# Kernel optimization log

Measured on AMD Instinct MI355X. Metric: run time of the kernel, lower is better.

Reference implementation:

```python
import jax, jax.numpy as jnp
import numpy as np

V, B, T, D, H = 32000, 64, 256, 512, 1024


def setup_inputs() -> dict:
    key = jax.random.key(0)
    ks = jax.random.split(key, 8)
    s = lambda i, shape: (jax.random.normal(ks[i], shape, jnp.float32) * 0.02)
    return {
        "y": jax.random.randint(ks[0], (B, T), 0, V),
        "hidden": jnp.zeros((B, H), jnp.float32),
        "emb_table": s(1, (V, D)),
        "Wx": s(2, (D, 3 * H)),
        "Wh": s(3, (H, 3 * H)),
        "bx": jnp.zeros((3 * H,), jnp.float32),
        "bh": jnp.zeros((3 * H,), jnp.float32),
        "W_out": s(4, (H, D)),
        "b_out": jnp.zeros((D,), jnp.float32),
    }


def _gru_step(h, x, Wx, Wh, bx, bh):
    # PyTorch GRUCell semantics: r,z gates, candidate n with r gating the
    # recurrent contribution (including its bias term).
    gx = x @ Wx + bx          # [B, 3H]
    gh = h @ Wh + bh          # [B, 3H]
    xr, xz, xn = jnp.split(gx, 3, axis=-1)
    hr, hz, hn = jnp.split(gh, 3, axis=-1)
    r = jax.nn.sigmoid(xr + hr)
    z = jax.nn.sigmoid(xz + hz)
    n = jnp.tanh(xn + r * hn)
    return (1.0 - z) * n + z * h


def reference(y, hidden, emb_table, Wx, Wh, bx, bh, W_out, b_out):
    emb = emb_table[y]                       # [B, T, D] token embedding lookup

    def step(h, x_t):                        # x_t: [B, D]
        h2 = _gru_step(h, x_t, Wx, Wh, bx, bh)
        return h2, h2

    _, outs = jax.lax.scan(step, hidden, jnp.swapaxes(emb, 0, 1))  # [T, B, H]
    out = jnp.swapaxes(outs, 0, 1)           # [B, T, H] decoder hiddens
    logits = jnp.tanh(out @ W_out + b_out)   # [B, T, D]; dropout_rate=0 -> identity
    return logits
```

## Files before the change

### kernel.cpp

```cpp
#include <hip/hip_runtime.h>
#include <stdint.h>

typedef unsigned short u16;
typedef unsigned int u32;
typedef __attribute__((ext_vector_type(4))) unsigned int u32x4;
typedef __attribute__((ext_vector_type(4))) float f32x4;
typedef __attribute__((ext_vector_type(8))) __bf16 bf16x8;

#define MFMA16(a, b, c) __builtin_amdgcn_mfma_f32_16x16x32_bf16((a), (b), (c), 0, 0, 0)

__device__ __forceinline__ u16 f2b(float f) {
  union { float f; unsigned u; } v; v.f = f;
  unsigned r = v.u + 0x7FFFu + ((v.u >> 16) & 1u);
  return (u16)(r >> 16);
}
__device__ __forceinline__ float b2f(u16 h) {
  union { unsigned u; float f; } v; v.u = ((unsigned)h) << 16;
  return v.f;
}
__device__ __forceinline__ float sigm(float x) { return 1.0f / (1.0f + __expf(-x)); }
__device__ __forceinline__ float tanh_fast(float x) {
  x = fminf(fmaxf(x, -15.0f), 15.0f);
  float t = __expf(2.0f * x);
  return (t - 1.0f) / (t + 1.0f);
}

template <int OFF>
__device__ __forceinline__ u32x4 ld16_sc(const void* p) {
  u32x4 r;
  asm volatile("global_load_dwordx4 %0, %1, off offset:%2 sc0 sc1"
               : "=v"(r) : "v"(p), "i"(OFF));
  return r;
}
__device__ __forceinline__ void st16_sc(void* p, u32x4 v) {
  asm volatile("global_store_dwordx4 %0, %1, off sc0 sc1"
               :: "v"(p), "v"(v) : "memory");
}
__device__ __forceinline__ void st4_sc(u32* p, u32 v) {
  asm volatile("global_store_dword %0, %1, off sc0 sc1"
               :: "v"(p), "v"(v) : "memory");
}
__device__ __forceinline__ u32 ld4_sc(const u32* p) {
  u32 r;
  asm volatile("global_load_dword %0, %1, off sc0 sc1\n\t"
               "s_waitcnt vmcnt(0)"
               : "=v"(r) : "v"(p) : "memory");
  return r;
}


__global__ void transpose_cvt(const float* __restrict__ src, u16* __restrict__ dst,
                              int R, int C) {
  __shared__ float tile[32][33];
  const int c0 = blockIdx.x * 32, r0 = blockIdx.y * 32;
  const int tx = threadIdx.x, ty = threadIdx.y;
  for (int i = ty; i < 32; i += 8)
    tile[i][tx] = src[(size_t)(r0 + i) * C + (c0 + tx)];
  __syncthreads();
  for (int i = ty; i < 32; i += 8)
    dst[(size_t)(c0 + i) * R + (r0 + tx)] = f2b(tile[tx][i]);
}

__global__ void gather_cast(const int* __restrict__ y, const float* __restrict__ tab,
                            u16* __restrict__ A) {
  const int idx = blockIdx.x * 256 + threadIdx.x;
  const int m = idx >> 7;
  const int d0 = (idx & 127) << 2;
  const float4 v = *reinterpret_cast<const float4*>(tab + (size_t)y[m] * 512 + d0);
  ushort4 o;
  o.x = f2b(v.x); o.y = f2b(v.y); o.z = f2b(v.z); o.w = f2b(v.w);
  *reinterpret_cast<ushort4*>(A + (size_t)m * 512 + d0) = o;
}

__global__ void cast_h0_blocked(const float* __restrict__ h, u16* __restrict__ dst) {
  const int i = blockIdx.x * 256 + threadIdx.x;
  const int b = i >> 10, n = i & 1023;
  const int r = b >> 4, ii = b & 15, g = n >> 4, j = n & 15;
  dst[((size_t)r * 64 + g) * 256 + ii * 16 + j] = f2b(h[(size_t)b * 1024 + n]);
}

template <int EPI>
__global__ __launch_bounds__(256, 2) void gemm_bt(
    const u16* __restrict__ A, const u16* __restrict__ Bt,
    const float* __restrict__ bias, void* __restrict__ Cout,
    int M, int N, int K) {
  __shared__ u16 As[4096], Bs[4096];
  const int tid = threadIdx.x, lane = tid & 63, w = tid >> 6;
  const int wm = w >> 1, wn = w & 1, c = lane & 15, hq = lane >> 4;
  const int m0 = blockIdx.y * 128, n0 = blockIdx.x * 128;
  f32x4 acc[4][4] = {};

  const int slot0 = tid, slot1 = 256 + tid;
  const int r0_ = slot0 >> 2, ko0 = (slot0 & 3) << 3;
  const int r1_ = slot1 >> 2, ko1 = (slot1 & 3) << 3;

  for (int k0 = 0; k0 < K; k0 += 32) {
    const u32x4 a0 = *(const u32x4*)(A + (size_t)(m0 + r0_) * K + k0 + ko0);
    const u32x4 a1 = *(const u32x4*)(A + (size_t)(m0 + r1_) * K + k0 + ko1);
    const u32x4 b0 = *(const u32x4*)(Bt + (size_t)(n0 + r0_) * K + k0 + ko0);
    const u32x4 b1 = *(const u32x4*)(Bt + (size_t)(n0 + r1_) * K + k0 + ko1);
    __syncthreads();
    *(u32x4*)(As + r0_ * 32 + ko0) = a0;
    *(u32x4*)(As + r1_ * 32 + ko1) = a1;
    *(u32x4*)(Bs + r0_ * 32 + ko0) = b0;
    *(u32x4*)(Bs + r1_ * 32 + ko1) = b1;
    __syncthreads();
    u32x4 af[4], bf[4];
#pragma unroll
    for (int i = 0; i < 4; ++i) {
      af[i] = *(const u32x4*)(As + (wm * 64 + i * 16 + c) * 32 + hq * 8);
      bf[i] = *(const u32x4*)(Bs + (wn * 64 + i * 16 + c) * 32 + hq * 8);
    }
#pragma unroll
    for (int mi = 0; mi < 4; ++mi)
#pragma unroll
      for (int ni = 0; ni < 4; ++ni)
        acc[mi][ni] = MFMA16(__builtin_bit_cast(bf16x8, af[mi]),
                             __builtin_bit_cast(bf16x8, bf[ni]), acc[mi][ni]);
  }

#pragma unroll
  for (int ni = 0; ni < 4; ++ni) {
    const int col = n0 + wn * 64 + ni * 16 + c;
    const float bv = bias[col];
#pragma unroll
    for (int mi = 0; mi < 4; ++mi) {
#pragma unroll
      for (int i = 0; i < 4; ++i) {
        const int m = m0 + wm * 64 + mi * 16 + hq * 4 + i;
        const float v = acc[mi][ni][i] + bv;
        if (EPI == 0) {
          const int dr = (m & 255) * 64 + (m >> 8);
          ((u16*)Cout)[(size_t)dr * N + col] = f2b(v);
        } else {
          const int dr = (m & 63) * 256 + (m >> 6);
          ((float*)Cout)[(size_t)dr * N + col] = tanh_fast(v);
        }
      }
    }
  }
}

__global__ __launch_bounds__(320, 1) void scan_kernel(
    const u16* __restrict__ wh_t,
    const float* __restrict__ bh,
    const float* __restrict__ h0,
    const u16* __restrict__ gx,
    u16* __restrict__ hbuf,
    u16* __restrict__ outs,
    u32* __restrict__ tags) {
  __shared__ u16 whs[96 * 512];
  __shared__ float red[2][4][3][256];
  __shared__ __align__(16) u16 htile[16][16];
  const int g = blockIdx.x >> 2, r = blockIdx.x & 3;
  const int tid = threadIdx.x, lane = tid & 63, s = tid >> 6;
  const int c = lane & 15, hq = lane >> 4;
  const int gcol = g * 16 + c;
  const int row0 = r * 16;

  for (int fb = s; fb < 96; fb += 5) {
    const int ss = fb / 24, kk = (fb % 24) / 3, ct = fb % 3;
    const int n = ct * 1024 + g * 16 + c;
    const int k = ss * 256 + kk * 32 + hq * 8;
    *(u32x4*)(whs + fb * 512 + lane * 8) =
        *(const u32x4*)(wh_t + (size_t)n * 1024 + k);
  }
  float bhv[3], hprev[4];
  u16 gxr[4][3];
  if (s == 4) {
#pragma unroll
    for (int ct = 0; ct < 3; ++ct) bhv[ct] = bh[ct * 1024 + gcol];
#pragma unroll
    for (int i = 0; i < 4; ++i)
      hprev[i] = h0[(size_t)(row0 + hq * 4 + i) * 1024 + gcol];
    const u16* gp = gx + gcol;
#pragma unroll
    for (int i = 0; i < 4; ++i) {
      const int b = row0 + hq * 4 + i;
      gxr[i][0] = gp[(size_t)b * 3072];
      gxr[i][1] = gp[(size_t)b * 3072 + 1024];
      gxr[i][2] = gp[(size_t)b * 3072 + 2048];
    }
  }
  __syncthreads();

  for (int t = 0; t < 256; ++t) {
    if (s < 4) {
      if (t > 0 && lane < 16) {
        const u32* tp = tags + (((size_t)(t & 1) * 4 + r) * 64 + s * 16 + lane) * 32;
        while (__ballot(ld4_sc(tp) < (u32)t)) {}
      }

      u32x4 af[8];
      {
        const u16* ap0 = hbuf + (((size_t)(t & 1) * 4 + r) * 64 + s * 16 + (hq >> 1)) * 256 +
                         c * 16 + (hq & 1) * 8;
        const u16* ap1 = ap0 + 2048;
        af[0] = ld16_sc<0>(ap0);    af[1] = ld16_sc<1024>(ap0);
        af[2] = ld16_sc<2048>(ap0); af[3] = ld16_sc<3072>(ap0);
        af[4] = ld16_sc<0>(ap1);    af[5] = ld16_sc<1024>(ap1);
        af[6] = ld16_sc<2048>(ap1); af[7] = ld16_sc<3072>(ap1);
      }
      asm volatile("s_waitcnt vmcnt(0)" ::: "memory");
      __builtin_amdgcn_sched_barrier(0);

      f32x4 acc[3] = {};
#pragma unroll
      for (int kk = 0; kk < 8; ++kk) {
        const int fb = (s * 8 + kk) * 3;
        const u32x4 b0 = *(const u32x4*)(whs + (fb + 0) * 512 + lane * 8);
        const u32x4 b1 = *(const u32x4*)(whs + (fb + 1) * 512 + lane * 8);
        const u32x4 b2 = *(const u32x4*)(whs + (fb + 2) * 512 + lane * 8);
        const bf16x8 a = __builtin_bit_cast(bf16x8, af[kk]);
        acc[0] = MFMA16(a, __builtin_bit_cast(bf16x8, b0), acc[0]);
        acc[1] = MFMA16(a, __builtin_bit_cast(bf16x8, b1), acc[1]);
        acc[2] = MFMA16(a, __builtin_bit_cast(bf16x8, b2), acc[2]);
      }
#pragma unroll
      for (int ct = 0; ct < 3; ++ct)
        *(f32x4*)&red[t & 1][s][ct][lane * 4] = acc[ct];
    }
    __syncthreads();

    if (s == 4) {
      f32x4 a0 = {}, a1 = {}, a2 = {};
#pragma unroll
      for (int j = 0; j < 4; ++j) {
        a0 += *(const f32x4*)&red[t & 1][j][0][lane * 4];
        a1 += *(const f32x4*)&red[t & 1][j][1][lane * 4];
        a2 += *(const f32x4*)&red[t & 1][j][2][lane * 4];
      }
#pragma unroll
      for (int i = 0; i < 4; ++i) {
        const float xr = b2f(gxr[i][0]);
        const float xz = b2f(gxr[i][1]);
        const float xn = b2f(gxr[i][2]);
        const float rr = sigm(xr + a0[i] + bhv[0]);
        const float zz = sigm(xz + a1[i] + bhv[1]);
        const float nn = tanh_fast(xn + rr * (a2[i] + bhv[2]));
        const float hnew = (1.0f - zz) * nn + zz * hprev[i];
        hprev[i] = hnew;
        htile[hq * 4 + i][c] = f2b(hnew);
      }
      asm volatile("s_waitcnt lgkmcnt(0)" ::: "memory");
      __builtin_amdgcn_sched_barrier(0);
      u32x4 hv;
      if (lane < 32) {
        hv = *(const u32x4*)((const u16*)htile + lane * 8);
        st16_sc(hbuf + (((size_t)((t + 1) & 1) * 4 + r) * 64 + g) * 256 + lane * 8, hv);
      }
      asm volatile("s_waitcnt vmcnt(0)" ::: "memory");
      if (lane == 0)
        st4_sc(tags + (((size_t)((t + 1) & 1) * 4 + r) * 64 + g) * 32, (u32)(t + 1));
      if (lane < 32) {
        const int row = row0 + (lane >> 1), c8 = (lane & 1) * 8;
        *(u32x4*)(outs + ((size_t)t * 64 + row) * 1024 + g * 16 + c8) = hv;
      }
      if (t < 255) {
        const u16* gp = gx + (size_t)(t + 1) * 64 * 3072 + gcol;
#pragma unroll
        for (int i = 0; i < 4; ++i) {
          const int b = row0 + hq * 4 + i;
          gxr[i][0] = gp[(size_t)b * 3072];
          gxr[i][1] = gp[(size_t)b * 3072 + 1024];
          gxr[i][2] = gp[(size_t)b * 3072 + 2048];
        }
      }
    }
  }
}

extern "C" void kernel_launch(void* const* d_in, const int* in_sizes, int n_in,
                              void* d_out, int out_size, void* d_ws, size_t ws_size,
                              hipStream_t stream) {
  (void)in_sizes; (void)n_in; (void)out_size; (void)ws_size;
  const int* y = (const int*)d_in[0];
  const float* hidden = (const float*)d_in[1];
  const float* emb = (const float*)d_in[2];
  const float* Wx = (const float*)d_in[3];
  const float* Wh = (const float*)d_in[4];
  const float* bx = (const float*)d_in[5];
  const float* bh = (const float*)d_in[6];
  const float* Wout = (const float*)d_in[7];
  const float* bout = (const float*)d_in[8];

  char* p = (char*)d_ws;
  u16* wx_t = (u16*)p; p += (size_t)3072 * 512 * 2;
  u16* wh_t = (u16*)p; p += (size_t)3072 * 1024 * 2;
  u16* wo_t = (u16*)p; p += (size_t)512 * 1024 * 2;
  u16* aemb = (u16*)p; p += (size_t)16384 * 512 * 2;
  u16* gx   = (u16*)p; p += (size_t)16384 * 3072 * 2;
  u16* outs = (u16*)p; p += (size_t)16384 * 1024 * 2;
  u16* hbuf = (u16*)p; p += (size_t)2 * 4 * 64 * 256 * 2;
  u32* tags = (u32*)p;

  hipMemsetAsync(tags, 0, 2 * 4 * 64 * 32 * sizeof(u32), stream);
  transpose_cvt<<<dim3(96, 16), dim3(32, 8), 0, stream>>>(Wx, wx_t, 512, 3072);
  transpose_cvt<<<dim3(96, 32), dim3(32, 8), 0, stream>>>(Wh, wh_t, 1024, 3072);
  transpose_cvt<<<dim3(16, 32), dim3(32, 8), 0, stream>>>(Wout, wo_t, 1024, 512);
  gather_cast<<<dim3(8192), dim3(256), 0, stream>>>(y, emb, aemb);
  cast_h0_blocked<<<dim3(256), dim3(256), 0, stream>>>(hidden, hbuf);

  gemm_bt<0><<<dim3(24, 128), dim3(256), 0, stream>>>(aemb, wx_t, bx, (void*)gx,
                                                      16384, 3072, 512);
  scan_kernel<<<dim3(256), dim3(320), 0, stream>>>(wh_t, bh, hidden, gx,
                                                   hbuf, outs, tags);
  gemm_bt<1><<<dim3(4, 128), dim3(256), 0, stream>>>(outs, wo_t, bout,
                                                     d_out, 16384, 512, 1024);
}
```

Before: 934.8 us.

## Keep full hidden history in blocked hbuf, drop separate outs copy, pipeline tag polling

The scan now writes each step's hidden state to a per-timestep slot in a 257-deep blocked buffer instead of a double buffer. This removes the extra row-major store to outs, and the output GEMM reads the blocked layout directly through a new A-layout template path. Tag polling keeps two outstanding loads in flight, and h-tile reads use plain loads instead of cache-bypassing asm loads. The cost is a larger workspace and a more complex address computation in the output GEMM. Plain loads may return stale cached data, although each slot is written only once.

```diff
diff --git a/kernel.cpp b/kernel.cpp
--- a/kernel.cpp
+++ b/kernel.cpp
@@ -25,13 +25,6 @@
   return (t - 1.0f) / (t + 1.0f);
 }
 
-template <int OFF>
-__device__ __forceinline__ u32x4 ld16_sc(const void* p) {
-  u32x4 r;
-  asm volatile("global_load_dwordx4 %0, %1, off offset:%2 sc0 sc1"
-               : "=v"(r) : "v"(p), "i"(OFF));
-  return r;
-}
 __device__ __forceinline__ void st16_sc(void* p, u32x4 v) {
   asm volatile("global_store_dwordx4 %0, %1, off sc0 sc1"
                :: "v"(p), "v"(v) : "memory");
@@ -39,13 +32,6 @@
 __device__ __forceinline__ void st4_sc(u32* p, u32 v) {
   asm volatile("global_store_dword %0, %1, off sc0 sc1"
                :: "v"(p), "v"(v) : "memory");
-}
-__device__ __forceinline__ u32 ld4_sc(const u32* p) {
-  u32 r;
-  asm volatile("global_load_dword %0, %1, off sc0 sc1\n\t"
-               "s_waitcnt vmcnt(0)"
-               : "=v"(r) : "v"(p) : "memory");
-  return r;
 }
 
 
@@ -79,7 +65,7 @@
   dst[((size_t)r * 64 + g) * 256 + ii * 16 + j] = f2b(h[(size_t)b * 1024 + n]);
 }
 
-template <int EPI>
+template <int EPI, int ALAYOUT>
 __global__ __launch_bounds__(256, 2) void gemm_bt(
     const u16* __restrict__ A, const u16* __restrict__ Bt,
     const float* __restrict__ bias, void* __restrict__ Cout,
@@ -95,8 +81,17 @@
   const int r1_ = slot1 >> 2, ko1 = (slot1 & 3) << 3;
 
   for (int k0 = 0; k0 < K; k0 += 32) {
-    const u32x4 a0 = *(const u32x4*)(A + (size_t)(m0 + r0_) * K + k0 + ko0);
-    const u32x4 a1 = *(const u32x4*)(A + (size_t)(m0 + r1_) * K + k0 + ko1);
+    u32x4 a0, a1;
+    if (ALAYOUT == 0) {
+      a0 = *(const u32x4*)(A + (size_t)(m0 + r0_) * K + k0 + ko0);
+      a1 = *(const u32x4*)(A + (size_t)(m0 + r1_) * K + k0 + ko1);
+    } else {
+      const int ma = m0 + r0_, ka = k0 + ko0, mb = m0 + r1_, kb = k0 + ko1;
+      a0 = *(const u32x4*)(A + ((((size_t)(ma >> 6) + 1) * 4 + ((ma >> 4) & 3)) * 64 +
+                                (ka >> 4)) * 256 + (ma & 15) * 16 + (ka & 15));
+      a1 = *(const u32x4*)(A + ((((size_t)(mb >> 6) + 1) * 4 + ((mb >> 4) & 3)) * 64 +
+                                (kb >> 4)) * 256 + (mb & 15) * 16 + (kb & 15));
+    }
     const u32x4 b0 = *(const u32x4*)(Bt + (size_t)(n0 + r0_) * K + k0 + ko0);
     const u32x4 b1 = *(const u32x4*)(Bt + (size_t)(n0 + r1_) * K + k0 + ko1);
     __syncthreads();
@@ -147,7 +142,6 @@
     const float* __restrict__ h0,
     const u16* __restrict__ gx,
     u16* __restrict__ hbuf,
-    u16* __restrict__ outs,
     u32* __restrict__ tags) {
   __shared__ u16 whs[96 * 512];
   __shared__ float red[2][4][3][256];
@@ -186,23 +180,37 @@
 
   for (int t = 0; t < 256; ++t) {
     if (s < 4) {
-      if (t > 0 && lane < 16) {
-        const u32* tp = tags + (((size_t)(t & 1) * 4 + r) * 64 + s * 16 + lane) * 32;
-        while (__ballot(ld4_sc(tp) < (u32)t)) {}
+      if (t > 0) {
+        const u32* tp = tags + ((size_t)(t & 1) * 4 + r) * (64 * 32) +
+                        (s * 16 + (lane & 15)) * 32;
+        u32 v0, v1;
+        asm volatile("global_load_dword %0, %1, off sc0 sc1" : "=v"(v0) : "v"(tp));
+        asm volatile("global_load_dword %0, %1, off sc0 sc1" : "=v"(v1) : "v"(tp));
+        while (true) {
+          asm volatile("s_waitcnt vmcnt(1)" ::: "memory");
+          if (!__ballot(v0 < (u32)t)) break;
+          asm volatile("global_load_dword %0, %1, off sc0 sc1" : "=v"(v0) : "v"(tp));
+          asm volatile("s_waitcnt vmcnt(1)" ::: "memory");
+          if (!__ballot(v1 < (u32)t)) break;
+          asm volatile("global_load_dword %0, %1, off sc0 sc1" : "=v"(v1) : "v"(tp));
+        }
+        asm volatile("s_waitcnt vmcnt(0)" ::: "memory");
       }
 
       u32x4 af[8];
       {
-        const u16* ap0 = hbuf + (((size_t)(t & 1) * 4 + r) * 64 + s * 16 + (hq >> 1)) * 256 +
-                         c * 16 + (hq & 1) * 8;
+        const u16* ap0 = hbuf + ((size_t)t * 4 + r) * 16384 +
+                         (s * 16 + (hq >> 1)) * 256 + c * 16 + (hq & 1) * 8;
         const u16* ap1 = ap0 + 2048;
-        af[0] = ld16_sc<0>(ap0);    af[1] = ld16_sc<1024>(ap0);
-        af[2] = ld16_sc<2048>(ap0); af[3] = ld16_sc<3072>(ap0);
-        af[4] = ld16_sc<0>(ap1);    af[5] = ld16_sc<1024>(ap1);
-        af[6] = ld16_sc<2048>(ap1); af[7] = ld16_sc<3072>(ap1);
-      }
-      asm volatile("s_waitcnt vmcnt(0)" ::: "memory");
-      __builtin_amdgcn_sched_barrier(0);
+        af[0] = *(const u32x4*)(ap0);
+        af[1] = *(const u32x4*)(ap0 + 512);
+        af[2] = *(const u32x4*)(ap0 + 1024);
+        af[3] = *(const u32x4*)(ap0 + 1536);
+        af[4] = *(const u32x4*)(ap1);
+        af[5] = *(const u32x4*)(ap1 + 512);
+        af[6] = *(const u32x4*)(ap1 + 1024);
+        af[7] = *(const u32x4*)(ap1 + 1536);
+      }
 
       f32x4 acc[3] = {};
 #pragma unroll
@@ -244,18 +252,14 @@
       }
       asm volatile("s_waitcnt lgkmcnt(0)" ::: "memory");
       __builtin_amdgcn_sched_barrier(0);
-      u32x4 hv;
       if (lane < 32) {
-        hv = *(const u32x4*)((const u16*)htile + lane * 8);
-        st16_sc(hbuf + (((size_t)((t + 1) & 1) * 4 + r) * 64 + g) * 256 + lane * 8, hv);
+        const u32x4 hv = *(const u32x4*)((const u16*)htile + lane * 8);
+        st16_sc(hbuf + ((size_t)(t + 1) * 4 + r) * 16384 + g * 256 + lane * 8, hv);
       }
       asm volatile("s_waitcnt vmcnt(0)" ::: "memory");
       if (lane == 0)
-        st4_sc(tags + (((size_t)((t + 1) & 1) * 4 + r) * 64 + g) * 32, (u32)(t + 1));
-      if (lane < 32) {
-        const int row = row0 + (lane >> 1), c8 = (lane & 1) * 8;
-        *(u32x4*)(outs + ((size_t)t * 64 + row) * 1024 + g * 16 + c8) = hv;
-      }
+        st4_sc(tags + ((size_t)((t + 1) & 1) * 4 + r) * (64 * 32) + g * 32,
+               (u32)(t + 1));
       if (t < 255) {
         const u16* gp = gx + (size_t)(t + 1) * 64 * 3072 + gcol;
 #pragma unroll
@@ -290,8 +294,7 @@
   u16* wo_t = (u16*)p; p += (size_t)512 * 1024 * 2;
   u16* aemb = (u16*)p; p += (size_t)16384 * 512 * 2;
   u16* gx   = (u16*)p; p += (size_t)16384 * 3072 * 2;
-  u16* outs = (u16*)p; p += (size_t)16384 * 1024 * 2;
-  u16* hbuf = (u16*)p; p += (size_t)2 * 4 * 64 * 256 * 2;
+  u16* hbuf = (u16*)p; p += (size_t)257 * 4 * 64 * 256 * 2;
   u32* tags = (u32*)p;
 
   hipMemsetAsync(tags, 0, 2 * 4 * 64 * 32 * sizeof(u32), stream);
@@ -301,10 +304,10 @@
   gather_cast<<<dim3(8192), dim3(256), 0, stream>>>(y, emb, aemb);
   cast_h0_blocked<<<dim3(256), dim3(256), 0, stream>>>(hidden, hbuf);
 
-  gemm_bt<0><<<dim3(24, 128), dim3(256), 0, stream>>>(aemb, wx_t, bx, (void*)gx,
-                                                      16384, 3072, 512);
+  gemm_bt<0, 0><<<dim3(24, 128), dim3(256), 0, stream>>>(aemb, wx_t, bx, (void*)gx,
+                                                         16384, 3072, 512);
   scan_kernel<<<dim3(256), dim3(320), 0, stream>>>(wh_t, bh, hidden, gx,
-                                                   hbuf, outs, tags);
-  gemm_bt<1><<<dim3(4, 128), dim3(256), 0, stream>>>(outs, wo_t, bout,
-                                                     d_out, 16384, 512, 1024);
-}
+                                                   hbuf, tags);
+  gemm_bt<1, 1><<<dim3(4, 128), dim3(256), 0, stream>>>(hbuf, wo_t, bout,
+                                                        d_out, 16384, 512, 1024);
+}
```

Result: slower. 1.057 ms (+13.1%).

## Fuse prep kernels, stream GEMM tiles via global_load_lds, drop outs buffer

Applied to the files above, without the earlier changes.

Merges the three transposes, the embedding gather, the h0 cast and the tag memset into one prep kernel, which removes several launches. The GEMM now copies tiles from global memory straight into LDS with global_load_lds instead of staging them through registers. The scan writes every timestep's hidden state into a 257-slot blocked history buffer rather than a double buffer plus a separate outs array. The output GEMM reads that blocked layout directly, so the extra outs store is gone from the serial recurrence, at the cost of more complex address math and a larger workspace.

```diff
diff --git a/kernel.cpp b/kernel.cpp
--- a/kernel.cpp
+++ b/kernel.cpp
@@ -48,38 +48,61 @@
   return r;
 }
 
-
-__global__ void transpose_cvt(const float* __restrict__ src, u16* __restrict__ dst,
-                              int R, int C) {
+__device__ __forceinline__ void gld_lds16(const void* g, void* l) {
+  __builtin_amdgcn_global_load_lds(
+      (const __attribute__((address_space(1))) void*)(g),
+      (__attribute__((address_space(3))) void*)(l), 16, 0, 0);
+}
+
+__global__ __launch_bounds__(256) void prep_all(
+    const float* __restrict__ Wx, const float* __restrict__ Wh,
+    const float* __restrict__ Wout, const int* __restrict__ y,
+    const float* __restrict__ emb, const float* __restrict__ hidden,
+    u16* __restrict__ wx_t, u16* __restrict__ wh_t, u16* __restrict__ wo_t,
+    u16* __restrict__ aemb, u16* __restrict__ hbuf, u32* __restrict__ tags) {
   __shared__ float tile[32][33];
-  const int c0 = blockIdx.x * 32, r0 = blockIdx.y * 32;
-  const int tx = threadIdx.x, ty = threadIdx.y;
-  for (int i = ty; i < 32; i += 8)
-    tile[i][tx] = src[(size_t)(r0 + i) * C + (c0 + tx)];
-  __syncthreads();
-  for (int i = ty; i < 32; i += 8)
-    dst[(size_t)(c0 + i) * R + (r0 + tx)] = f2b(tile[tx][i]);
-}
-
-__global__ void gather_cast(const int* __restrict__ y, const float* __restrict__ tab,
-                            u16* __restrict__ A) {
-  const int idx = blockIdx.x * 256 + threadIdx.x;
-  const int m = idx >> 7;
-  const int d0 = (idx & 127) << 2;
-  const float4 v = *reinterpret_cast<const float4*>(tab + (size_t)y[m] * 512 + d0);
-  ushort4 o;
-  o.x = f2b(v.x); o.y = f2b(v.y); o.z = f2b(v.z); o.w = f2b(v.w);
-  *reinterpret_cast<ushort4*>(A + (size_t)m * 512 + d0) = o;
-}
-
-__global__ void cast_h0_blocked(const float* __restrict__ h, u16* __restrict__ dst) {
-  const int i = blockIdx.x * 256 + threadIdx.x;
-  const int b = i >> 10, n = i & 1023;
-  const int r = b >> 4, ii = b & 15, g = n >> 4, j = n & 15;
-  dst[((size_t)r * 64 + g) * 256 + ii * 16 + j] = f2b(h[(size_t)b * 1024 + n]);
-}
-
-template <int EPI>
+  const int b = blockIdx.x, tid = threadIdx.x;
+  const int tx = tid & 31, ty = tid >> 5;
+
+  const float* src = nullptr; u16* dst = nullptr; int R = 0, C = 0, tb = 0;
+  if (b < 1536)      { src = Wx;   dst = wx_t; R = 512;  C = 3072; tb = b; }
+  else if (b < 4608) { src = Wh;   dst = wh_t; R = 1024; C = 3072; tb = b - 1536; }
+  else if (b < 5120) { src = Wout; dst = wo_t; R = 1024; C = 512;  tb = b - 4608; }
+
+  if (src) {
+    const int xt = C >> 5;
+    const int c0 = (tb % xt) * 32, r0 = (tb / xt) * 32;
+    for (int i = ty; i < 32; i += 8)
+      tile[i][tx] = src[(size_t)(r0 + i) * C + (c0 + tx)];
+    __syncthreads();
+    for (int i = ty; i < 32; i += 8)
+      dst[(size_t)(c0 + i) * R + (r0 + tx)] = f2b(tile[tx][i]);
+    return;
+  }
+  if (b < 13312) {
+    const int idx = (b - 5120) * 256 + tid;
+    const int m = idx >> 7, d0 = (idx & 127) << 2;
+    const float4 v = *reinterpret_cast<const float4*>(emb + (size_t)y[m] * 512 + d0);
+    ushort4 o;
+    o.x = f2b(v.x); o.y = f2b(v.y); o.z = f2b(v.z); o.w = f2b(v.w);
+    *reinterpret_cast<ushort4*>(aemb + (size_t)m * 512 + d0) = o;
+    return;
+  }
+  if (b < 13568) {
+    const int i = (b - 13312) * 256 + tid;
+    const int bb = i >> 10, n = i & 1023;
+    const int r = bb >> 4, ii = bb & 15, g = n >> 4, j = n & 15;
+    hbuf[((size_t)r * 64 + g) * 256 + ii * 16 + j] = f2b(hidden[(size_t)bb * 1024 + n]);
+    return;
+  }
+  {
+    const int base = ((b - 13568) * 256 + tid) * 8;
+#pragma unroll
+    for (int q = 0; q < 8; ++q) tags[base + q] = 0;
+  }
+}
+
+template <int EPI, int ALAYOUT>
 __global__ __launch_bounds__(256, 2) void gemm_bt(
     const u16* __restrict__ A, const u16* __restrict__ Bt,
     const float* __restrict__ bias, void* __restrict__ Cout,
@@ -90,20 +113,28 @@
   const int m0 = blockIdx.y * 128, n0 = blockIdx.x * 128;
   f32x4 acc[4][4] = {};
 
-  const int slot0 = tid, slot1 = 256 + tid;
-  const int r0_ = slot0 >> 2, ko0 = (slot0 & 3) << 3;
-  const int r1_ = slot1 >> 2, ko1 = (slot1 & 3) << 3;
+  const int r0_ = tid >> 2, ko0 = (tid & 3) << 3;
+  const int r1_ = (256 + tid) >> 2, ko1 = ((256 + tid) & 3) << 3;
 
   for (int k0 = 0; k0 < K; k0 += 32) {
-    const u32x4 a0 = *(const u32x4*)(A + (size_t)(m0 + r0_) * K + k0 + ko0);
-    const u32x4 a1 = *(const u32x4*)(A + (size_t)(m0 + r1_) * K + k0 + ko1);
-    const u32x4 b0 = *(const u32x4*)(Bt + (size_t)(n0 + r0_) * K + k0 + ko0);
-    const u32x4 b1 = *(const u32x4*)(Bt + (size_t)(n0 + r1_) * K + k0 + ko1);
+    const u16 *ga0, *ga1;
+    if (ALAYOUT == 0) {
+      ga0 = A + (size_t)(m0 + r0_) * K + k0 + ko0;
+      ga1 = A + (size_t)(m0 + r1_) * K + k0 + ko1;
+    } else {
+      const int ma = m0 + r0_, ka = k0 + ko0, mb = m0 + r1_, kb = k0 + ko1;
+      ga0 = A + ((((size_t)(ma >> 6) + 1) * 4 + ((ma >> 4) & 3)) * 64 +
+                 (ka >> 4)) * 256 + (ma & 15) * 16 + (ka & 15);
+      ga1 = A + ((((size_t)(mb >> 6) + 1) * 4 + ((mb >> 4) & 3)) * 64 +
+                 (kb >> 4)) * 256 + (mb & 15) * 16 + (kb & 15);
+    }
+    const u16* gb0 = Bt + (size_t)(n0 + r0_) * K + k0 + ko0;
+    const u16* gb1 = Bt + (size_t)(n0 + r1_) * K + k0 + ko1;
     __syncthreads();
-    *(u32x4*)(As + r0_ * 32 + ko0) = a0;
-    *(u32x4*)(As + r1_ * 32 + ko1) = a1;
-    *(u32x4*)(Bs + r0_ * 32 + ko0) = b0;
-    *(u32x4*)(Bs + r1_ * 32 + ko1) = b1;
+    gld_lds16(ga0, (char*)As + tid * 16);
+    gld_lds16(ga1, (char*)As + 4096 + tid * 16);
+    gld_lds16(gb0, (char*)Bs + tid * 16);
+    gld_lds16(gb1, (char*)Bs + 4096 + tid * 16);
     __syncthreads();
     u32x4 af[4], bf[4];
 #pragma unroll
@@ -147,7 +178,6 @@
     const float* __restrict__ h0,
     const u16* __restrict__ gx,
     u16* __restrict__ hbuf,
-    u16* __restrict__ outs,
     u32* __restrict__ tags) {
   __shared__ u16 whs[96 * 512];
   __shared__ float red[2][4][3][256];
@@ -193,8 +223,8 @@
 
       u32x4 af[8];
       {
-        const u16* ap0 = hbuf + (((size_t)(t & 1) * 4 + r) * 64 + s * 16 + (hq >> 1)) * 256 +
-                         c * 16 + (hq & 1) * 8;
+        const u16* ap0 = hbuf + ((size_t)t * 4 + r) * 16384 +
+                         (s * 16 + (hq >> 1)) * 256 + c * 16 + (hq & 1) * 8;
         const u16* ap1 = ap0 + 2048;
         af[0] = ld16_sc<0>(ap0);    af[1] = ld16_sc<1024>(ap0);
         af[2] = ld16_sc<2048>(ap0); af[3] = ld16_sc<3072>(ap0);
@@ -244,18 +274,13 @@
       }
       asm volatile("s_waitcnt lgkmcnt(0)" ::: "memory");
       __builtin_amdgcn_sched_barrier(0);
-      u32x4 hv;
       if (lane < 32) {
-        hv = *(const u32x4*)((const u16*)htile + lane * 8);
-        st16_sc(hbuf + (((size_t)((t + 1) & 1) * 4 + r) * 64 + g) * 256 + lane * 8, hv);
+        const u32x4 hv = *(const u32x4*)((const u16*)htile + lane * 8);
+        st16_sc(hbuf + ((size_t)(t + 1) * 4 + r) * 16384 + g * 256 + lane * 8, hv);
       }
       asm volatile("s_waitcnt vmcnt(0)" ::: "memory");
       if (lane == 0)
         st4_sc(tags + (((size_t)((t + 1) & 1) * 4 + r) * 64 + g) * 32, (u32)(t + 1));
-      if (lane < 32) {
-        const int row = row0 + (lane >> 1), c8 = (lane & 1) * 8;
-        *(u32x4*)(outs + ((size_t)t * 64 + row) * 1024 + g * 16 + c8) = hv;
-      }
       if (t < 255) {
         const u16* gp = gx + (size_t)(t + 1) * 64 * 3072 + gcol;
 #pragma unroll
@@ -290,21 +315,16 @@
   u16* wo_t = (u16*)p; p += (size_t)512 * 1024 * 2;
   u16* aemb = (u16*)p; p += (size_t)16384 * 512 * 2;
   u16* gx   = (u16*)p; p += (size_t)16384 * 3072 * 2;
-  u16* outs = (u16*)p; p += (size_t)16384 * 1024 * 2;
-  u16* hbuf = (u16*)p; p += (size_t)2 * 4 * 64 * 256 * 2;
+  u16* hbuf = (u16*)p; p += (size_t)257 * 4 * 64 * 256 * 2;
   u32* tags = (u32*)p;
 
-  hipMemsetAsync(tags, 0, 2 * 4 * 64 * 32 * sizeof(u32), stream);
-  transpose_cvt<<<dim3(96, 16), dim3(32, 8), 0, stream>>>(Wx, wx_t, 512, 3072);
-  transpose_cvt<<<dim3(96, 32), dim3(32, 8), 0, stream>>>(Wh, wh_t, 1024, 3072);
-  transpose_cvt<<<dim3(16, 32), dim3(32, 8), 0, stream>>>(Wout, wo_t, 1024, 512);
-  gather_cast<<<dim3(8192), dim3(256), 0, stream>>>(y, emb, aemb);
-  cast_h0_blocked<<<dim3(256), dim3(256), 0, stream>>>(hidden, hbuf);
-
-  gemm_bt<0><<<dim3(24, 128), dim3(256), 0, stream>>>(aemb, wx_t, bx, (void*)gx,
-                                                      16384, 3072, 512);
+  prep_all<<<dim3(13600), dim3(256), 0, stream>>>(Wx, Wh, Wout, y, emb, hidden,
+                                                  wx_t, wh_t, wo_t, aemb, hbuf,
+                                                  tags);
+  gemm_bt<0, 0><<<dim3(24, 128), dim3(256), 0, stream>>>(aemb, wx_t, bx, (void*)gx,
+                                                         16384, 3072, 512);
   scan_kernel<<<dim3(256), dim3(320), 0, stream>>>(wh_t, bh, hidden, gx,
-                                                   hbuf, outs, tags);
-  gemm_bt<1><<<dim3(4, 128), dim3(256), 0, stream>>>(outs, wo_t, bout,
-                                                     d_out, 16384, 512, 1024);
-}
+                                                   hbuf, tags);
+  gemm_bt<1, 1><<<dim3(4, 128), dim3(256), 0, stream>>>(hbuf, wo_t, bout,
+                                                        d_out, 16384, 512, 1024);
+}
```

New measurement: 876.9 us (median of 2 runs). -6.2%, faster.
